# Kernel tuning notes

Hardware: AMD Instinct MI355X
Metric: run time of the kernel (lower is better)

## Reference

```python
import jax, jax.numpy as jnp
import numpy as np

DELTA = 1.0
EPS = 1e-8  # torch CosineSimilarity eps


def setup_inputs() -> dict:
    key = jax.random.key(0)
    k1, k2, k3, k4 = jax.random.split(key, 4)
    N1, N2, D, C = 4096, 4096, 256, 16
    return {
        "mmd1": jax.random.normal(k1, (N1, D), dtype=jnp.float32),
        "mmd2": jax.random.normal(k2, (N2, D), dtype=jnp.float32),
        "label1": jax.random.randint(k3, (N1,), 0, C, dtype=jnp.int64),
        "label2": jax.random.randint(k4, (N2,), 0, C, dtype=jnp.int64),
    }


def reference(mmd1, mmd2, label1, label2):
    # Normalize rows with torch-style eps clamp: x / max(||x||, eps)
    n1 = mmd1 / jnp.maximum(jnp.linalg.norm(mmd1, axis=1, keepdims=True), EPS)
    n2 = mmd2 / jnp.maximum(jnp.linalg.norm(mmd2, axis=1, keepdims=True), EPS)
    cos = jnp.einsum("id,jd->ij", n1, n2)  # [N1, N2] pairwise cosine
    same = label1[:, None] == label2[None, :]  # [N1, N2] bool
    per_pair = jnp.where(same, jnp.maximum(DELTA - cos, 0.0), cos)
    return jnp.mean(per_pair)
```

## Files before the change

### kernel.cpp

```cpp
#include <hip/hip_runtime.h>
#include <hip/hip_bf16.h>
#include <cstdint>

#define N1 4096
#define N2 4096
#define DD 256
#define DELTA 1.0f
#define EPSN 1e-8f

#define BM 128
#define BN 128
#define BK 32

typedef __attribute__((ext_vector_type(8))) __bf16 bf16x8;
typedef __attribute__((ext_vector_type(4))) float f32x4;

typedef const __attribute__((address_space(1))) void* gptr_t;
typedef __attribute__((address_space(3))) void* lptr_t;

__global__ __launch_bounds__(256) void normalize_kernel(
    const float* __restrict__ mmd1, const float* __restrict__ mmd2,
    ushort* __restrict__ out1, ushort* __restrict__ out2,
    float* __restrict__ ws_sum)
{
    int row = blockIdx.x;
    const float* src;
    ushort* dst;
    if (row < N1) { src = mmd1 + (size_t)row * DD;        dst = out1 + (size_t)row * DD; }
    else          { src = mmd2 + (size_t)(row - N1) * DD; dst = out2 + (size_t)(row - N1) * DD; }

    int t = threadIdx.x;
    float x = src[t];
    float ss = x * x;
    #pragma unroll
    for (int off = 32; off; off >>= 1) ss += __shfl_down(ss, off, 64);
    __shared__ float wsum[4];
    int wid = t >> 6, lane = t & 63;
    if (lane == 0) wsum[wid] = ss;
    __syncthreads();
    float tot = wsum[0] + wsum[1] + wsum[2] + wsum[3];
    float scale = 1.0f / fmaxf(sqrtf(tot), EPSN);
    __hip_bfloat16 b = __float2bfloat16(x * scale);
    dst[t] = *reinterpret_cast<const ushort*>(&b);

    if (row == 0 && t == 0) ws_sum[0] = 0.0f;
}

__global__ __launch_bounds__(256) void cos_gemm_kernel(
    const ushort* __restrict__ A, const ushort* __restrict__ B,
    const int* __restrict__ lab1, const int* __restrict__ lab2,
    float* __restrict__ ws_sum)
{
    __shared__ __align__(16) ushort As[BM * BK];
    __shared__ __align__(16) ushort Bs[BN * BK];
    __shared__ int l1s[BM];
    __shared__ int l2s[BN];
    __shared__ float wredsum[4];

    const int row0 = blockIdx.y * BM;
    const int col0 = blockIdx.x * BN;
    const int t = threadIdx.x;
    const int lane = t & 63, wid = t >> 6;
    const int wr = wid >> 1, wc = wid & 1;

    if (t < BM) l1s[t] = lab1[row0 + t];
    else        l2s[t - BM] = lab2[col0 + (t - BM)];

    f32x4 acc[4][4] = {};

    for (int k0 = 0; k0 < DD; k0 += BK) {
        __syncthreads();
        #pragma unroll
        for (int it = 0; it < 2; ++it) {
            int t2 = t + it * 256;
            int r = t2 >> 2;
            int c = (t2 & 3) * 8;
            __builtin_amdgcn_global_load_lds(
                (gptr_t)(A + (size_t)(row0 + r) * DD + k0 + c),
                (lptr_t)(&As[r * BK + c]), 16, 0, 0);
            __builtin_amdgcn_global_load_lds(
                (gptr_t)(B + (size_t)(col0 + r) * DD + k0 + c),
                (lptr_t)(&Bs[r * BK + c]), 16, 0, 0);
        }
        __syncthreads();

        bf16x8 af[4], bfr[4];
        const int krow = (lane >> 4) * 8;
        const int rsel = lane & 15;
        #pragma unroll
        for (int m = 0; m < 4; ++m)
            af[m] = *reinterpret_cast<const bf16x8*>(&As[(wr * 64 + m * 16 + rsel) * BK + krow]);
        #pragma unroll
        for (int n = 0; n < 4; ++n)
            bfr[n] = *reinterpret_cast<const bf16x8*>(&Bs[(wc * 64 + n * 16 + rsel) * BK + krow]);
        #pragma unroll
        for (int m = 0; m < 4; ++m)
            #pragma unroll
            for (int n = 0; n < 4; ++n)
                acc[m][n] = __builtin_amdgcn_mfma_f32_16x16x32_bf16(af[m], bfr[n], acc[m][n], 0, 0, 0);
    }

    float lsum = 0.0f;
    const int csel = lane & 15;
    const int rbase = (lane >> 4) * 4;
    #pragma unroll
    for (int n = 0; n < 4; ++n) {
        int j = wc * 64 + n * 16 + csel;
        int l2 = l2s[j];
        #pragma unroll
        for (int m = 0; m < 4; ++m) {
            #pragma unroll
            for (int e = 0; e < 4; ++e) {
                int i = wr * 64 + m * 16 + rbase + e;
                float cosv = acc[m][n][e];
                float v = (l1s[i] == l2) ? fmaxf(DELTA - cosv, 0.0f) : cosv;
                lsum += v;
            }
        }
    }
    #pragma unroll
    for (int off = 32; off; off >>= 1) lsum += __shfl_down(lsum, off, 64);
    if (lane == 0) wredsum[wid] = lsum;
    __syncthreads();
    if (t == 0) atomicAdd(ws_sum, wredsum[0] + wredsum[1] + wredsum[2] + wredsum[3]);
}

__global__ void finalize_kernel(const float* __restrict__ ws_sum, float* __restrict__ out) {
    out[0] = ws_sum[0] * (1.0f / ((float)N1 * (float)N2));
}

extern "C" void kernel_launch(void* const* d_in, const int* in_sizes, int n_in,
                              void* d_out, int out_size, void* d_ws, size_t ws_size,
                              hipStream_t stream) {
    const float* mmd1 = (const float*)d_in[0];
    const float* mmd2 = (const float*)d_in[1];
    const int* lab1 = (const int*)d_in[2];
    const int* lab2 = (const int*)d_in[3];

    ushort* n1b = (ushort*)d_ws;
    ushort* n2b = n1b + (size_t)N1 * DD;
    float* ws_sum = (float*)((char*)d_ws + (size_t)(N1 + N2) * DD * 2);
    float* out = (float*)d_out;

    normalize_kernel<<<N1 + N2, 256, 0, stream>>>(mmd1, mmd2, n1b, n2b, ws_sum);
    cos_gemm_kernel<<<dim3(BN / 4, BM / 4) , 256, 0, stream>>>(n1b, n2b, lab1, lab2, ws_sum);
    finalize_kernel<<<1, 1, 0, stream>>>(ws_sum, out);
}
```

Measured before the change: 93.59 us.

## Vectorize row normalization, double K tile, and XOR-swizzle LDS layout in GEMM

After: 87.95 us. -6.0%, faster.

```diff
diff --git a/kernel.cpp b/kernel.cpp
--- a/kernel.cpp
+++ b/kernel.cpp
@@ -10,7 +10,7 @@
 
 #define BM 128
 #define BN 128
-#define BK 32
+#define BK 64
 
 typedef __attribute__((ext_vector_type(8))) __bf16 bf16x8;
 typedef __attribute__((ext_vector_type(4))) float f32x4;
@@ -23,27 +23,32 @@
     ushort* __restrict__ out1, ushort* __restrict__ out2,
     float* __restrict__ ws_sum)
 {
-    int row = blockIdx.x;
-    const float* src;
-    ushort* dst;
-    if (row < N1) { src = mmd1 + (size_t)row * DD;        dst = out1 + (size_t)row * DD; }
-    else          { src = mmd2 + (size_t)(row - N1) * DD; dst = out2 + (size_t)(row - N1) * DD; }
+    const int wid = threadIdx.x >> 6, lane = threadIdx.x & 63;
+    const int row = blockIdx.x * 4 + wid;
 
-    int t = threadIdx.x;
-    float x = src[t];
-    float ss = x * x;
+    const float* srcp;
+    ushort* dstp;
+    if (row < N1) { srcp = mmd1 + (size_t)row * DD;        dstp = out1 + (size_t)row * DD; }
+    else          { srcp = mmd2 + (size_t)(row - N1) * DD; dstp = out2 + (size_t)(row - N1) * DD; }
+
+    float4 v = reinterpret_cast<const float4*>(srcp)[lane];
+    float ss = v.x * v.x + v.y * v.y + v.z * v.z + v.w * v.w;
     #pragma unroll
-    for (int off = 32; off; off >>= 1) ss += __shfl_down(ss, off, 64);
-    __shared__ float wsum[4];
-    int wid = t >> 6, lane = t & 63;
-    if (lane == 0) wsum[wid] = ss;
-    __syncthreads();
-    float tot = wsum[0] + wsum[1] + wsum[2] + wsum[3];
-    float scale = 1.0f / fmaxf(sqrtf(tot), EPSN);
-    __hip_bfloat16 b = __float2bfloat16(x * scale);
-    dst[t] = *reinterpret_cast<const ushort*>(&b);
+    for (int off = 32; off; off >>= 1) ss += __shfl_xor(ss, off, 64);
+    float scale = 1.0f / fmaxf(sqrtf(ss), EPSN);
 
-    if (row == 0 && t == 0) ws_sum[0] = 0.0f;
+    __hip_bfloat16 b0 = __float2bfloat16(v.x * scale);
+    __hip_bfloat16 b1 = __float2bfloat16(v.y * scale);
+    __hip_bfloat16 b2 = __float2bfloat16(v.z * scale);
+    __hip_bfloat16 b3 = __float2bfloat16(v.w * scale);
+    ushort4 o;
+    o.x = *reinterpret_cast<const ushort*>(&b0);
+    o.y = *reinterpret_cast<const ushort*>(&b1);
+    o.z = *reinterpret_cast<const ushort*>(&b2);
+    o.w = *reinterpret_cast<const ushort*>(&b3);
+    reinterpret_cast<ushort4*>(dstp)[lane] = o;
+
+    if (blockIdx.x == 0 && threadIdx.x == 0) ws_sum[0] = 0.0f;
 }
 
 __global__ __launch_bounds__(256) void cos_gemm_kernel(
@@ -71,49 +76,56 @@
     for (int k0 = 0; k0 < DD; k0 += BK) {
         __syncthreads();
         #pragma unroll
-        for (int it = 0; it < 2; ++it) {
-            int t2 = t + it * 256;
-            int r = t2 >> 2;
-            int c = (t2 & 3) * 8;
+        for (int it = 0; it < 4; ++it) {
+            int idx = t + it * 256;
+            int r = idx >> 3;
+            int c = idx & 7;
+            int gc = c ^ (r & 7);
             __builtin_amdgcn_global_load_lds(
-                (gptr_t)(A + (size_t)(row0 + r) * DD + k0 + c),
-                (lptr_t)(&As[r * BK + c]), 16, 0, 0);
+                (gptr_t)(A + (size_t)(row0 + r) * DD + k0 + gc * 8),
+                (lptr_t)(&As[r * BK + c * 8]), 16, 0, 0);
             __builtin_amdgcn_global_load_lds(
-                (gptr_t)(B + (size_t)(col0 + r) * DD + k0 + c),
-                (lptr_t)(&Bs[r * BK + c]), 16, 0, 0);
+                (gptr_t)(B + (size_t)(col0 + r) * DD + k0 + gc * 8),
+                (lptr_t)(&Bs[r * BK + c * 8]), 16, 0, 0);
         }
         __syncthreads();
 
-        bf16x8 af[4], bfr[4];
-        const int krow = (lane >> 4) * 8;
-        const int rsel = lane & 15;
         #pragma unroll
-        for (int m = 0; m < 4; ++m)
-            af[m] = *reinterpret_cast<const bf16x8*>(&As[(wr * 64 + m * 16 + rsel) * BK + krow]);
-        #pragma unroll
-        for (int n = 0; n < 4; ++n)
-            bfr[n] = *reinterpret_cast<const bf16x8*>(&Bs[(wc * 64 + n * 16 + rsel) * BK + krow]);
-        #pragma unroll
-        for (int m = 0; m < 4; ++m)
+        for (int kk = 0; kk < 2; ++kk) {
+            const int ck = kk * 4 + (lane >> 4);
+            const int rsel = lane & 15;
+            bf16x8 af[4], bfr[4];
             #pragma unroll
-            for (int n = 0; n < 4; ++n)
-                acc[m][n] = __builtin_amdgcn_mfma_f32_16x16x32_bf16(af[m], bfr[n], acc[m][n], 0, 0, 0);
+            for (int m = 0; m < 4; ++m) {
+                int R = wr * 64 + m * 16 + rsel;
+                af[m] = *reinterpret_cast<const bf16x8*>(&As[R * BK + (ck ^ (R & 7)) * 8]);
+            }
+            #pragma unroll
+            for (int n = 0; n < 4; ++n) {
+                int R = wc * 64 + n * 16 + rsel;
+                bfr[n] = *reinterpret_cast<const bf16x8*>(&Bs[R * BK + (ck ^ (R & 7)) * 8]);
+            }
+            #pragma unroll
+            for (int m = 0; m < 4; ++m)
+                #pragma unroll
+                for (int n = 0; n < 4; ++n)
+                    acc[m][n] = __builtin_amdgcn_mfma_f32_16x16x32_bf16(af[m], bfr[n], acc[m][n], 0, 0, 0);
+        }
     }
 
     float lsum = 0.0f;
     const int csel = lane & 15;
-    const int rbase = (lane >> 4) * 4;
     #pragma unroll
     for (int n = 0; n < 4; ++n) {
         int j = wc * 64 + n * 16 + csel;
         int l2 = l2s[j];
         #pragma unroll
         for (int m = 0; m < 4; ++m) {
+            int ibase = wr * 64 + m * 16 + (lane >> 4) * 4;
             #pragma unroll
             for (int e = 0; e < 4; ++e) {
-                int i = wr * 64 + m * 16 + rbase + e;
                 float cosv = acc[m][n][e];
-                float v = (l1s[i] == l2) ? fmaxf(DELTA - cosv, 0.0f) : cosv;
+                float v = (l1s[ibase + e] == l2) ? fmaxf(DELTA - cosv, 0.0f) : cosv;
                 lsum += v;
             }
         }
@@ -142,7 +154,7 @@
     float* ws_sum = (float*)((char*)d_ws + (size_t)(N1 + N2) * DD * 2);
     float* out = (float*)d_out;
 
-    normalize_kernel<<<N1 + N2, 256, 0, stream>>>(mmd1, mmd2, n1b, n2b, ws_sum);
-    cos_gemm_kernel<<<dim3(BN / 4, BM / 4) , 256, 0, stream>>>(n1b, n2b, lab1, lab2, ws_sum);
+    normalize_kernel<<<(N1 + N2) / 4, 256, 0, stream>>>(mmd1, mmd2, n1b, n2b, ws_sum);
+    cos_gemm_kernel<<<dim3(N2 / BN, N1 / BM), 256, 0, stream>>>(n1b, n2b, lab1, lab2, ws_sum);
     finalize_kernel<<<1, 1, 0, stream>>>(ws_sum, out);
 }
```
